# Kernel optimization log

Measured on AMD Instinct MI355X. Metric: run time of the kernel, lower is better.

Reference implementation:

```python
import jax, jax.numpy as jnp
import numpy as np

H = 8          # num_attention_heads
HEAD_DIM = 24  # 192 / 8


def setup_inputs() -> dict:
    key = jax.random.key(0)
    k1, k2, k3 = jax.random.split(key, 3)
    B, S, D = 4, 2048, 192
    x = jax.random.normal(k1, (B, S, D), dtype=jnp.float32)
    mask0 = jnp.zeros((B, 1, 1, S), dtype=jnp.float32)  # HF additive attention mask
    w_attn = jax.random.normal(k2, (D, 3 * D), dtype=jnp.float32) * 0.02
    b_attn = jnp.zeros((3 * D,), dtype=jnp.float32)
    w_proj = jax.random.normal(k3, (D, D), dtype=jnp.float32) * 0.02
    b_proj = jnp.zeros((D,), dtype=jnp.float32)
    return {"x": x, "mask0": mask0, "w_attn": w_attn, "b_attn": b_attn,
            "w_proj": w_proj, "b_proj": b_proj}


def reference(x, mask0, w_attn, b_attn, w_proj, b_proj):
    B, S, D = x.shape
    # fused QKV projection (GPT2 Conv1D: x @ W + b)
    qkv = x @ w_attn + b_attn                       # [B,S,3D]
    q, k, v = jnp.split(qkv, 3, axis=-1)
    def split_heads(t):
        return t.reshape(B, S, H, HEAD_DIM).transpose(0, 2, 1, 3)  # [B,H,S,hd]
    q, k, v = split_heads(q), split_heads(k), split_heads(v)
    # scaled QK^T
    scores = jnp.einsum('bhqd,bhkd->bhqk', q, k) / jnp.sqrt(
        jnp.asarray(HEAD_DIM, dtype=q.dtype))
    # causal mask (masked_fill with dtype min), then additive padding mask
    causal = jnp.tril(jnp.ones((S, S), dtype=bool))
    mask_value = jnp.finfo(scores.dtype).min
    scores = jnp.where(causal, scores, mask_value) + mask0
    attn = jax.nn.softmax(scores, axis=-1)          # [B,H,S,S]
    # attn_dropout is identity in eval mode
    out = jnp.einsum('bhqk,bhkd->bhqd', attn, v)    # [B,H,S,hd]
    out = out.transpose(0, 2, 1, 3).reshape(B, S, D)
    return out @ w_proj + b_proj
```

## Files before the change

### kernel.cpp

```cpp
#include <hip/hip_runtime.h>

typedef unsigned short u16;
typedef unsigned int u32;
typedef __bf16 bf16x8 __attribute__((ext_vector_type(8)));
typedef float f32x4 __attribute__((ext_vector_type(4)));
typedef float f32x16 __attribute__((ext_vector_type(16)));
typedef u32 u32x2 __attribute__((ext_vector_type(2)));
typedef u32 u32x4 __attribute__((ext_vector_type(4)));

#define NB 4
#define NS 2048
#define ND 192
#define NH 8
#define HD 24
#define NM (NB*NS)
#define N3 (3*ND)
#define NBH (NB*NH)
#define NROWS (NBH*NS)

#define LOG2E 1.4426950408889634f
#define QSCALE (0.20412414523193152f * 1.4426950408889634f)

__device__ __forceinline__ u16 f2bf(float f){
  union { float f; unsigned u; } a; a.f = f;
  unsigned r = a.u + 0x7fffu + ((a.u >> 16) & 1u);
  return (u16)(r >> 16);
}
__device__ __forceinline__ float b2f(u16 h){
  union { u32 u; float f; } a; a.u = ((u32)h) << 16; return a.f;
}
__device__ __forceinline__ u32 cvtpk(float lo, float hi){
  u32 r; asm("v_cvt_pk_bf16_f32 %0, %1, %2" : "=v"(r) : "v"(lo), "v"(hi)); return r;
}
__device__ __forceinline__ void pswap(u32 &a, u32 &b){
  asm("v_permlane32_swap_b32 %0, %1" : "+v"(a), "+v"(b));
}

__device__ __forceinline__ void transpose64(
    const float* __restrict__ src, int srcN, u16* __restrict__ dst, int dstK,
    int k0, int n0, u16 (*sh)[68], int tid)
{
  int r = tid >> 2, cs = tid & 3;
  const float* sp = src + (size_t)(k0 + r)*srcN + n0 + cs*16;
  #pragma unroll
  for (int q = 0; q < 4; ++q) {
    float4 v = *(const float4*)(sp + q*4);
    u16 o[4] = { f2bf(v.x), f2bf(v.y), f2bf(v.z), f2bf(v.w) };
    *(u32x2*)&sh[r][cs*16 + q*4] = *(const u32x2*)o;
  }
  __syncthreads();
  int n = tid >> 2, ks = tid & 3;
  u16 tmp[16];
  #pragma unroll
  for (int j = 0; j < 16; ++j) tmp[j] = sh[ks*16 + j][n];
  u16* dp = dst + (size_t)(n0 + n)*dstK + k0 + ks*16;
  *(u32x4*)dp       = *(const u32x4*)tmp;
  *(u32x4*)(dp + 8) = *(const u32x4*)(tmp + 8);
}

__global__ __launch_bounds__(256) void prep_kernel(
    const float* __restrict__ w_attn, const float* __restrict__ w_proj,
    u16* __restrict__ wta, u16* __restrict__ wtp)
{
  __shared__ u16 sh[64][68];
  const int bid = blockIdx.x, tid = threadIdx.x;
  if (bid < 27) {
    int kt = bid/9, nt = bid%9;
    transpose64(w_attn, N3, wta, ND, kt*64, nt*64, sh, tid);
  } else {
    int t = bid - 27; int kt = t/3, nt = t%3;
    transpose64(w_proj, ND, wtp, ND, kt*64, nt*64, sh, tid);
  }
}

__global__ __launch_bounds__(256) void qkv_kernel(
    const float* __restrict__ x, const u16* __restrict__ wta,
    const float* __restrict__ b_attn, const float* __restrict__ mask0,
    u16* __restrict__ qp, u16* __restrict__ kp, u16* __restrict__ vtp)
{
  __shared__ u16 tile[96*72];
  const int m0 = blockIdx.x*64, n0 = blockIdx.y*96;
  const int tid = threadIdx.x;
  const int w = tid >> 6, lane = tid & 63, c = lane & 15, g = lane >> 4;
  f32x4 acc[6] = {};
  const int ar = m0 + w*16 + c;
  const float* xrow = x + (size_t)ar*ND;
  #pragma unroll
  for (int ks = 0; ks < 6; ++ks) {
    float4 xa = *(const float4*)(xrow + ks*32 + g*8);
    float4 xc = *(const float4*)(xrow + ks*32 + g*8 + 4);
    union { u32 wrd[4]; bf16x8 v; } afu;
    afu.wrd[0] = cvtpk(xa.x, xa.y); afu.wrd[1] = cvtpk(xa.z, xa.w);
    afu.wrd[2] = cvtpk(xc.x, xc.y); afu.wrd[3] = cvtpk(xc.z, xc.w);
    bf16x8 af = afu.v;
    #pragma unroll
    for (int t = 0; t < 6; ++t) {
      bf16x8 bfr = *(const bf16x8*)(wta + (size_t)(n0 + t*16 + c)*ND + ks*32 + g*8);
      acc[t] = __builtin_amdgcn_mfma_f32_16x16x32_bf16(af, bfr, acc[t], 0, 0, 0);
    }
  }
  const int b = m0 >> 11, sb = m0 & (NS-1);
  if (n0 >= 384) {
    const int h0 = (n0 - 384)/HD;
    #pragma unroll
    for (int t = 0; t < 6; ++t) {
      float bias = b_attn[n0 + t*16 + c];
      #pragma unroll
      for (int r = 0; r < 4; ++r)
        tile[(t*16 + c)*72 + w*16 + g*4 + r] = f2bf(acc[t][r] + bias);
    }
    __syncthreads();
    if (tid < 200) {
      int row = tid >> 1, seg = tid & 1;
      if (row < 96) {
        int hl = row / HD, dv = row % HD;
        u16* dst = vtp + ((size_t)((b*NH + h0 + hl)*32 + dv))*NS + sb + seg*32;
        const u16* src = &tile[row*72 + seg*32];
        #pragma unroll
        for (int q = 0; q < 4; ++q)
          *(u32x4*)(dst + q*8) = *(const u32x4*)(src + q*8);
      } else {
        int hl = row - 96;
        u16* dst = vtp + ((size_t)((b*NH + h0 + hl)*32 + 24))*NS + sb + seg*32;
        u16 ones[8] = {0x3F80,0x3F80,0x3F80,0x3F80,0x3F80,0x3F80,0x3F80,0x3F80};
        #pragma unroll
        for (int q = 0; q < 4; ++q)
          *(u32x4*)(dst + q*8) = *(const u32x4*)ones;
      }
    }
  } else {
    const bool isQ = (n0 < 192);
    const float scl = isQ ? QSCALE : 1.0f;
    #pragma unroll
    for (int t = 0; t < 6; ++t) {
      float bias = b_attn[n0 + t*16 + c];
      #pragma unroll
      for (int r = 0; r < 4; ++r)
        tile[(w*16 + g*4 + r)*104 + t*16 + c] = f2bf((acc[t][r] + bias)*scl);
    }
    __syncthreads();
    int row = tid >> 2, run = tid & 3;
    int h0 = (n0 % 192)/HD;
    u16 d24 = isQ ? (u16)0x3F80
                  : f2bf(mask0[b*NS + sb + row] * LOG2E);
    const u16* src = &tile[row*104 + run*24];
    union { u32x4 q[4]; u16 s[32]; } buf;
    buf.q[0] = *(const u32x4*)(src);
    buf.q[1] = *(const u32x4*)(src + 8);
    buf.q[2] = *(const u32x4*)(src + 16);
    buf.s[24] = d24;
    #pragma unroll
    for (int j = 25; j < 32; ++j) buf.s[j] = 0;
    u16* dst = (isQ ? qp : kp)
             + ((size_t)((b*NS + sb + row)*NH + h0 + run))*32;
    #pragma unroll
    for (int q = 0; q < 4; ++q)
      *(u32x4*)(dst + q*8) = buf.q[q];
  }
}

__global__ __launch_bounds__(256) void attn_kernel(
    const u16* __restrict__ qp, const u16* __restrict__ kp,
    const u16* __restrict__ vtp, u16* __restrict__ po, float* __restrict__ pmf)
{
  __shared__ u16 klds[2][64][40];
  __shared__ u16 vlds[2][32][72];

  const int bh = blockIdx.x;
  const int g  = 15 - (int)blockIdx.y;
  const int part = blockIdx.z;
  const int b = bh >> 3, h = bh & 7;
  const int tid = threadIdx.x;
  const int w = tid >> 6, lane = tid & 63, c = lane & 31, hi = lane >> 5;
  const int q0 = g*128 + w*32;
  const int t0 = part ? g + 1 : 0;
  const int ntp = g + 1;

  const size_t rowstride = NH*32;
  const size_t qkbase = (size_t)b*NS*rowstride + h*32;

  const u16* qrow = qp + qkbase + (size_t)(q0 + c)*rowstride;
  bf16x8 qf0 = *(const bf16x8*)(qrow + hi*8);
  bf16x8 qf1 = *(const bf16x8*)(qrow + 16 + hi*8);

  const int krow = tid >> 2, kch = tid & 3;
  const int vrow = tid >> 3, vch = tid & 7;
  const u16* kgsrc = kp + qkbase + (size_t)(t0*64 + krow)*rowstride + kch*8;
  const u16* vgsrc = vtp + ((size_t)(bh*32 + vrow))*NS + t0*64 + vch*8;

  u32x4 kreg = *(const u32x4*)(kgsrc);
  u32x4 vreg = *(const u32x4*)(vgsrc);
  *(u32x4*)&klds[0][krow][kch*8] = kreg;
  *(u32x4*)&vlds[0][vrow][vch*8] = vreg;
  __syncthreads();

  f32x16 o = {0};
  const f32x16 z16 = {0};
  float m = 0.f;

  for (int dt = 0; dt < ntp; ++dt) {
    const int cur = dt & 1;
    if (dt + 1 < ntp) {
      kreg = *(const u32x4*)(kgsrc + (size_t)(dt+1)*64*rowstride);
      vreg = *(const u32x4*)(vgsrc + (dt+1)*64);
    }
    const int kb0 = (t0 + dt)*64;
    if (kb0 <= q0) {
      const bool a1 = (kb0 + 32 <= q0);
      bf16x8 ka0 = *(const bf16x8*)&klds[cur][c][hi*8];
      bf16x8 ka1 = *(const bf16x8*)&klds[cur][c][16 + hi*8];
      __builtin_amdgcn_s_setprio(1);
      f32x16 st = __builtin_amdgcn_mfma_f32_32x32x16_bf16(ka0, qf0, z16, 0, 0, 0);
      st        = __builtin_amdgcn_mfma_f32_32x32x16_bf16(ka1, qf1, st,  0, 0, 0);
      __builtin_amdgcn_s_setprio(0);
      f32x16 su;
      if (a1) {
        bf16x8 kb0f = *(const bf16x8*)&klds[cur][32 + c][hi*8];
        bf16x8 kb1f = *(const bf16x8*)&klds[cur][32 + c][16 + hi*8];
        __builtin_amdgcn_s_setprio(1);
        su = __builtin_amdgcn_mfma_f32_32x32x16_bf16(kb0f, qf0, z16, 0, 0, 0);
        su = __builtin_amdgcn_mfma_f32_32x32x16_bf16(kb1f, qf1, su,  0, 0, 0);
        __builtin_amdgcn_s_setprio(0);
      }
      float pm = -3.0e38f;
      if (kb0 == q0) {
        #pragma unroll
        for (int r = 0; r < 16; ++r) {
          int krel = (r & 3) + 8*(r >> 2) + 4*hi;
          float s = (krel > c) ? -3.0e38f : st[r];
          st[r] = s; pm = fmaxf(pm, s);
        }
      } else {
        #pragma unroll
        for (int r = 0; r < 16; ++r) pm = fmaxf(pm, st[r]);
      }
      if (a1) {
        if (kb0 + 32 == q0) {
          #pragma unroll
          for (int r = 0; r < 16; ++r) {
            int krel = (r & 3) + 8*(r >> 2) + 4*hi;
            float s = (krel > c) ? -3.0e38f : su[r];
            su[r] = s; pm = fmaxf(pm, s);
          }
        } else {
          #pragma unroll
          for (int r = 0; r < 16; ++r) pm = fmaxf(pm, su[r]);
        }
      }
      if (!__all(pm - m <= 8.f)) {
        float pm2 = fmaxf(pm, __shfl_xor(pm, 32));
        float mn = fmaxf(m, pm2);
        float al = __builtin_amdgcn_exp2f(m - mn);
        #pragma unroll
        for (int r = 0; r < 16; ++r) o[r] *= al;
        m = mn;
      }
      #pragma unroll
      for (int r = 0; r < 16; ++r) st[r] = __builtin_amdgcn_exp2f(st[r] - m);
      if (a1) {
        #pragma unroll
        for (int r = 0; r < 16; ++r) su[r] = __builtin_amdgcn_exp2f(su[r] - m);
      }
      {
        u32 a0 = cvtpk(st[0], st[1]),  b0 = cvtpk(st[4], st[5]);
        u32 a1w = cvtpk(st[2], st[3]), b1 = cvtpk(st[6], st[7]);
        pswap(a0, b0); pswap(a1w, b1);
        u32 a2 = cvtpk(st[8], st[9]),  b2 = cvtpk(st[12], st[13]);
        u32 a3 = cvtpk(st[10], st[11]), b3 = cvtpk(st[14], st[15]);
        pswap(a2, b2); pswap(a3, b3);
        union { u32 wrd[4]; bf16x8 v; } pf0, pf1;
        pf0.wrd[0] = a0; pf0.wrd[1] = a1w; pf0.wrd[2] = b0; pf0.wrd[3] = b1;
        pf1.wrd[0] = a2; pf1.wrd[1] = a3;  pf1.wrd[2] = b2; pf1.wrd[3] = b3;
        bf16x8 va0 = *(const bf16x8*)&vlds[cur][c][hi*8];
        bf16x8 va1 = *(const bf16x8*)&vlds[cur][c][16 + hi*8];
        __builtin_amdgcn_s_setprio(1);
        o = __builtin_amdgcn_mfma_f32_32x32x16_bf16(va0, pf0.v, o, 0, 0, 0);
        o = __builtin_amdgcn_mfma_f32_32x32x16_bf16(va1, pf1.v, o, 0, 0, 0);
        __builtin_amdgcn_s_setprio(0);
      }
      if (a1) {
        u32 a0 = cvtpk(su[0], su[1]),  b0 = cvtpk(su[4], su[5]);
        u32 a1w = cvtpk(su[2], su[3]), b1 = cvtpk(su[6], su[7]);
        pswap(a0, b0); pswap(a1w, b1);
        u32 a2 = cvtpk(su[8], su[9]),  b2 = cvtpk(su[12], su[13]);
        u32 a3 = cvtpk(su[10], su[11]), b3 = cvtpk(su[14], su[15]);
        pswap(a2, b2); pswap(a3, b3);
        union { u32 wrd[4]; bf16x8 v; } pf0, pf1;
        pf0.wrd[0] = a0; pf0.wrd[1] = a1w; pf0.wrd[2] = b0; pf0.wrd[3] = b1;
        pf1.wrd[0] = a2; pf1.wrd[1] = a3;  pf1.wrd[2] = b2; pf1.wrd[3] = b3;
        bf16x8 va0 = *(const bf16x8*)&vlds[cur][c][32 + hi*8];
        bf16x8 va1 = *(const bf16x8*)&vlds[cur][c][48 + hi*8];
        __builtin_amdgcn_s_setprio(1);
        o = __builtin_amdgcn_mfma_f32_32x32x16_bf16(va0, pf0.v, o, 0, 0, 0);
        o = __builtin_amdgcn_mfma_f32_32x32x16_bf16(va1, pf1.v, o, 0, 0, 0);
        __builtin_amdgcn_s_setprio(0);
      }
    }
    if (dt + 1 < ntp) {
      *(u32x4*)&klds[cur^1][krow][kch*8] = kreg;
      *(u32x4*)&vlds[cur^1][vrow][vch*8] = vreg;
    }
    __syncthreads();
  }

  const int pidx = part*NROWS + bh*NS + q0 + c;
  u16* porow = po + (size_t)pidx*32;
  #pragma unroll
  for (int rr = 0; rr < 4; ++rr) {
    u32 lo = cvtpk(o[rr*4 + 0], o[rr*4 + 1]);
    u32 h2 = cvtpk(o[rr*4 + 2], o[rr*4 + 3]);
    u32x2 wv = {lo, h2};
    *(u32x2*)(porow + rr*8 + hi*4) = wv;
  }
  if (hi == 0) pmf[pidx] = (t0*64 <= q0) ? m : -3.0e38f;
}

__global__ __launch_bounds__(256) void merge_kernel(
    const u16* __restrict__ po, const float* __restrict__ pmf,
    u16* __restrict__ ao)
{
  int i = blockIdx.x*256 + threadIdx.x;
  int bh = i >> 11, q = i & (NS-1);
  int b = bh >> 3, h = bh & 7;
  float m1 = pmf[i], m2 = pmf[NROWS + i];
  float M = fmaxf(m1, m2);
  float w1 = __builtin_amdgcn_exp2f(m1 - M);
  float w2 = __builtin_amdgcn_exp2f(m2 - M);
  const u16* r1 = po + (size_t)i*32;
  const u16* r2 = r1 + (size_t)NROWS*32;
  u16 a1[32], a2[32];
  #pragma unroll
  for (int q4 = 0; q4 < 4; ++q4) {
    *(u32x4*)(a1 + q4*8) = *(const u32x4*)(r1 + q4*8);
    *(u32x4*)(a2 + q4*8) = *(const u32x4*)(r2 + q4*8);
  }
  float l = b2f(a1[24])*w1 + b2f(a2[24])*w2;
  float inv = 1.0f / l;
  u16 ob[24];
  #pragma unroll
  for (int d = 0; d < 24; ++d)
    ob[d] = f2bf((b2f(a1[d])*w1 + b2f(a2[d])*w2)*inv);
  u16* dst = ao + ((size_t)(b*NS + q))*ND + h*HD;
  #pragma unroll
  for (int q4 = 0; q4 < 3; ++q4)
    *(u32x4*)(dst + q4*8) = *(const u32x4*)(ob + q4*8);
}

__global__ __launch_bounds__(256) void proj_kernel(
    const u16* __restrict__ ao, const u16* __restrict__ wtp,
    const float* __restrict__ bp, float* __restrict__ out)
{
  const int m0 = blockIdx.x*64, n0 = blockIdx.y*64;
  const int tid = threadIdx.x;
  const int w = tid >> 6, lane = tid & 63, c = lane & 15, g = lane >> 4;
  f32x4 acc[4] = {};
  const int ar = m0 + w*16 + c;
  #pragma unroll
  for (int ks = 0; ks < 6; ++ks) {
    bf16x8 af = *(const bf16x8*)(ao + (size_t)ar*ND + ks*32 + g*8);
    #pragma unroll
    for (int t = 0; t < 4; ++t) {
      bf16x8 bfr = *(const bf16x8*)(wtp + (size_t)(n0 + t*16 + c)*ND + ks*32 + g*8);
      acc[t] = __builtin_amdgcn_mfma_f32_16x16x32_bf16(af, bfr, acc[t], 0, 0, 0);
    }
  }
  #pragma unroll
  for (int t = 0; t < 4; ++t) {
    int n = n0 + t*16 + c;
    float bias = bp[n];
    #pragma unroll
    for (int r = 0; r < 4; ++r) {
      int mm = m0 + w*16 + g*4 + r;
      out[(size_t)mm*ND + n] = acc[t][r] + bias;
    }
  }
}

extern "C" void kernel_launch(void* const* d_in, const int* in_sizes, int n_in,
                              void* d_out, int out_size, void* d_ws, size_t ws_size,
                              hipStream_t stream)
{
  const float* x      = (const float*)d_in[0];
  const float* mask0  = (const float*)d_in[1];
  const float* w_attn = (const float*)d_in[2];
  const float* b_attn = (const float*)d_in[3];
  const float* w_proj = (const float*)d_in[4];
  const float* b_proj = (const float*)d_in[5];
  float* out = (float*)d_out;

  char* ws = (char*)d_ws;
  u16*   qp  = (u16*)(ws);
  u16*   kp  = (u16*)(ws + ((size_t)4  << 20));
  u16*   vtp = (u16*)(ws + ((size_t)8  << 20));
  u16*   wta = (u16*)(ws + ((size_t)12 << 20));
  u16*   wtp = (u16*)(ws + ((size_t)12 << 20) + 256*1024);
  u16*   ao  = (u16*)(ws + ((size_t)12 << 20) + 512*1024);
  u16*   po  = (u16*)(ws + ((size_t)16 << 20));
  float* pmf = (float*)(ws + ((size_t)24 << 20));

  prep_kernel<<<36, 256, 0, stream>>>(w_attn, w_proj, wta, wtp);
  qkv_kernel<<<dim3(NM/64, 6), 256, 0, stream>>>(x, wta, b_attn, mask0,
                                                 qp, kp, vtp);
  attn_kernel<<<dim3(NBH, 16, 2), 256, 0, stream>>>(qp, kp, vtp, po, pmf);
  merge_kernel<<<256, 256, 0, stream>>>(po, pmf, ao);
  proj_kernel<<<dim3(NM/64, ND/64), 256, 0, stream>>>(ao, wtp, b_proj, out);
}
```

Before: 133.9 us.

## Split attention KV range into four balanced partitions and merge four partials

Each query block's causal key range is now divided evenly into four parts instead of two halves, and the attention grid launches four partitions along z. This gives more blocks and shorter per-block loops, aiming to improve load balance and occupancy across CUs. The merge kernel now combines four partial results with log-sum-exp weights. In exchange it adds more partial-output traffic and merge work, and some blocks with small g get no tiles and only write sentinel values.

New measurement: 133.9 us. No clear change (+0.0%).

```diff
diff --git a/kernel.cpp b/kernel.cpp
--- a/kernel.cpp
+++ b/kernel.cpp
@@ -17,6 +17,7 @@
 #define N3 (3*ND)
 #define NBH (NB*NH)
 #define NROWS (NBH*NS)
+#define NPART 4
 
 #define LOG2E 1.4426950408889634f
 #define QSCALE (0.20412414523193152f * 1.4426950408889634f)
@@ -173,8 +174,10 @@
   const int tid = threadIdx.x;
   const int w = tid >> 6, lane = tid & 63, c = lane & 31, hi = lane >> 5;
   const int q0 = g*128 + w*32;
-  const int t0 = part ? g + 1 : 0;
-  const int ntp = g + 1;
+  const int nt = 2*g + 2;
+  const int base = nt >> 2, rem = nt & 3;
+  const int cnt = base + (part < rem ? 1 : 0);
+  const int t0 = part*base + (part < rem ? part : rem);
 
   const size_t rowstride = NH*32;
   const size_t qkbase = (size_t)b*NS*rowstride + h*32;
@@ -188,119 +191,121 @@
   const u16* kgsrc = kp + qkbase + (size_t)(t0*64 + krow)*rowstride + kch*8;
   const u16* vgsrc = vtp + ((size_t)(bh*32 + vrow))*NS + t0*64 + vch*8;
 
-  u32x4 kreg = *(const u32x4*)(kgsrc);
-  u32x4 vreg = *(const u32x4*)(vgsrc);
-  *(u32x4*)&klds[0][krow][kch*8] = kreg;
-  *(u32x4*)&vlds[0][vrow][vch*8] = vreg;
-  __syncthreads();
-
   f32x16 o = {0};
   const f32x16 z16 = {0};
   float m = 0.f;
 
-  for (int dt = 0; dt < ntp; ++dt) {
-    const int cur = dt & 1;
-    if (dt + 1 < ntp) {
-      kreg = *(const u32x4*)(kgsrc + (size_t)(dt+1)*64*rowstride);
-      vreg = *(const u32x4*)(vgsrc + (dt+1)*64);
-    }
-    const int kb0 = (t0 + dt)*64;
-    if (kb0 <= q0) {
-      const bool a1 = (kb0 + 32 <= q0);
-      bf16x8 ka0 = *(const bf16x8*)&klds[cur][c][hi*8];
-      bf16x8 ka1 = *(const bf16x8*)&klds[cur][c][16 + hi*8];
-      __builtin_amdgcn_s_setprio(1);
-      f32x16 st = __builtin_amdgcn_mfma_f32_32x32x16_bf16(ka0, qf0, z16, 0, 0, 0);
-      st        = __builtin_amdgcn_mfma_f32_32x32x16_bf16(ka1, qf1, st,  0, 0, 0);
-      __builtin_amdgcn_s_setprio(0);
-      f32x16 su;
-      if (a1) {
-        bf16x8 kb0f = *(const bf16x8*)&klds[cur][32 + c][hi*8];
-        bf16x8 kb1f = *(const bf16x8*)&klds[cur][32 + c][16 + hi*8];
+  if (cnt > 0) {
+    u32x4 kreg = *(const u32x4*)(kgsrc);
+    u32x4 vreg = *(const u32x4*)(vgsrc);
+    *(u32x4*)&klds[0][krow][kch*8] = kreg;
+    *(u32x4*)&vlds[0][vrow][vch*8] = vreg;
+    __syncthreads();
+
+    for (int dt = 0; dt < cnt; ++dt) {
+      const int cur = dt & 1;
+      if (dt + 1 < cnt) {
+        kreg = *(const u32x4*)(kgsrc + (size_t)(dt+1)*64*rowstride);
+        vreg = *(const u32x4*)(vgsrc + (dt+1)*64);
+      }
+      const int kb0 = (t0 + dt)*64;
+      if (kb0 <= q0) {
+        const bool a1 = (kb0 + 32 <= q0);
+        bf16x8 ka0 = *(const bf16x8*)&klds[cur][c][hi*8];
+        bf16x8 ka1 = *(const bf16x8*)&klds[cur][c][16 + hi*8];
         __builtin_amdgcn_s_setprio(1);
-        su = __builtin_amdgcn_mfma_f32_32x32x16_bf16(kb0f, qf0, z16, 0, 0, 0);
-        su = __builtin_amdgcn_mfma_f32_32x32x16_bf16(kb1f, qf1, su,  0, 0, 0);
+        f32x16 st = __builtin_amdgcn_mfma_f32_32x32x16_bf16(ka0, qf0, z16, 0, 0, 0);
+        st        = __builtin_amdgcn_mfma_f32_32x32x16_bf16(ka1, qf1, st,  0, 0, 0);
         __builtin_amdgcn_s_setprio(0);
-      }
-      float pm = -3.0e38f;
-      if (kb0 == q0) {
-        #pragma unroll
-        for (int r = 0; r < 16; ++r) {
-          int krel = (r & 3) + 8*(r >> 2) + 4*hi;
-          float s = (krel > c) ? -3.0e38f : st[r];
-          st[r] = s; pm = fmaxf(pm, s);
-        }
-      } else {
-        #pragma unroll
-        for (int r = 0; r < 16; ++r) pm = fmaxf(pm, st[r]);
-      }
-      if (a1) {
-        if (kb0 + 32 == q0) {
+        f32x16 su;
+        if (a1) {
+          bf16x8 kb0f = *(const bf16x8*)&klds[cur][32 + c][hi*8];
+          bf16x8 kb1f = *(const bf16x8*)&klds[cur][32 + c][16 + hi*8];
+          __builtin_amdgcn_s_setprio(1);
+          su = __builtin_amdgcn_mfma_f32_32x32x16_bf16(kb0f, qf0, z16, 0, 0, 0);
+          su = __builtin_amdgcn_mfma_f32_32x32x16_bf16(kb1f, qf1, su,  0, 0, 0);
+          __builtin_amdgcn_s_setprio(0);
+        }
+        float pm = -3.0e38f;
+        if (kb0 == q0) {
           #pragma unroll
           for (int r = 0; r < 16; ++r) {
             int krel = (r & 3) + 8*(r >> 2) + 4*hi;
-            float s = (krel > c) ? -3.0e38f : su[r];
-            su[r] = s; pm = fmaxf(pm, s);
+            float s = (krel > c) ? -3.0e38f : st[r];
+            st[r] = s; pm = fmaxf(pm, s);
           }
         } else {
           #pragma unroll
-          for (int r = 0; r < 16; ++r) pm = fmaxf(pm, su[r]);
+          for (int r = 0; r < 16; ++r) pm = fmaxf(pm, st[r]);
+        }
+        if (a1) {
+          if (kb0 + 32 == q0) {
+            #pragma unroll
+            for (int r = 0; r < 16; ++r) {
+              int krel = (r & 3) + 8*(r >> 2) + 4*hi;
+              float s = (krel > c) ? -3.0e38f : su[r];
+              su[r] = s; pm = fmaxf(pm, s);
+            }
+          } else {
+            #pragma unroll
+            for (int r = 0; r < 16; ++r) pm = fmaxf(pm, su[r]);
+          }
+        }
+        if (!__all(pm - m <= 8.f)) {
+          float pm2 = fmaxf(pm, __shfl_xor(pm, 32));
+          float mn = fmaxf(m, pm2);
+          float al = __builtin_amdgcn_exp2f(m - mn);
+          #pragma unroll
+          for (int r = 0; r < 16; ++r) o[r] *= al;
+          m = mn;
+        }
+        #pragma unroll
+        for (int r = 0; r < 16; ++r) st[r] = __builtin_amdgcn_exp2f(st[r] - m);
+        if (a1) {
+          #pragma unroll
+          for (int r = 0; r < 16; ++r) su[r] = __builtin_amdgcn_exp2f(su[r] - m);
+        }
+        {
+          u32 a0 = cvtpk(st[0], st[1]),  b0 = cvtpk(st[4], st[5]);
+          u32 a1w = cvtpk(st[2], st[3]), b1 = cvtpk(st[6], st[7]);
+          pswap(a0, b0); pswap(a1w, b1);
+          u32 a2 = cvtpk(st[8], st[9]),  b2 = cvtpk(st[12], st[13]);
+          u32 a3 = cvtpk(st[10], st[11]), b3 = cvtpk(st[14], st[15]);
+          pswap(a2, b2); pswap(a3, b3);
+          union { u32 wrd[4]; bf16x8 v; } pf0, pf1;
+          pf0.wrd[0] = a0; pf0.wrd[1] = a1w; pf0.wrd[2] = b0; pf0.wrd[3] = b1;
+          pf1.wrd[0] = a2; pf1.wrd[1] = a3;  pf1.wrd[2] = b2; pf1.wrd[3] = b3;
+          bf16x8 va0 = *(const bf16x8*)&vlds[cur][c][hi*8];
+          bf16x8 va1 = *(const bf16x8*)&vlds[cur][c][16 + hi*8];
+          __builtin_amdgcn_s_setprio(1);
+          o = __builtin_amdgcn_mfma_f32_32x32x16_bf16(va0, pf0.v, o, 0, 0, 0);
+          o = __builtin_amdgcn_mfma_f32_32x32x16_bf16(va1, pf1.v, o, 0, 0, 0);
+          __builtin_amdgcn_s_setprio(0);
+        }
+        if (a1) {
+          u32 a0 = cvtpk(su[0], su[1]),  b0 = cvtpk(su[4], su[5]);
+          u32 a1w = cvtpk(su[2], su[3]), b1 = cvtpk(su[6], su[7]);
+          pswap(a0, b0); pswap(a1w, b1);
+          u32 a2 = cvtpk(su[8], su[9]),  b2 = cvtpk(su[12], su[13]);
+          u32 a3 = cvtpk(su[10], su[11]), b3 = cvtpk(su[14], su[15]);
+          pswap(a2, b2); pswap(a3, b3);
+          union { u32 wrd[4]; bf16x8 v; } pf0, pf1;
+          pf0.wrd[0] = a0; pf0.wrd[1] = a1w; pf0.wrd[2] = b0; pf0.wrd[3] = b1;
+          pf1.wrd[0] = a2; pf1.wrd[1] = a3;  pf1.wrd[2] = b2; pf1.wrd[3] = b3;
+          bf16x8 va0 = *(const bf16x8*)&vlds[cur][c][32 + hi*8];
+          bf16x8 va1 = *(const bf16x8*)&vlds[cur][c][48 + hi*8];
+          __builtin_amdgcn_s_setprio(1);
+          o = __builtin_amdgcn_mfma_f32_32x32x16_bf16(va0, pf0.v, o, 0, 0, 0);
+          o = __builtin_amdgcn_mfma_f32_32x32x16_bf16(va1, pf1.v, o, 0, 0, 0);
+          __builtin_amdgcn_s_setprio(0);
         }
       }
-      if (!__all(pm - m <= 8.f)) {
-        float pm2 = fmaxf(pm, __shfl_xor(pm, 32));
-        float mn = fmaxf(m, pm2);
-        float al = __builtin_amdgcn_exp2f(m - mn);
-        #pragma unroll
-        for (int r = 0; r < 16; ++r) o[r] *= al;
-        m = mn;
+      if (dt + 1 < cnt) {
+        *(u32x4*)&klds[cur^1][krow][kch*8] = kreg;
+        *(u32x4*)&vlds[cur^1][vrow][vch*8] = vreg;
       }
-      #pragma unroll
-      for (int r = 0; r < 16; ++r) st[r] = __builtin_amdgcn_exp2f(st[r] - m);
-      if (a1) {
-        #pragma unroll
-        for (int r = 0; r < 16; ++r) su[r] = __builtin_amdgcn_exp2f(su[r] - m);
-      }
-      {
-        u32 a0 = cvtpk(st[0], st[1]),  b0 = cvtpk(st[4], st[5]);
-        u32 a1w = cvtpk(st[2], st[3]), b1 = cvtpk(st[6], st[7]);
-        pswap(a0, b0); pswap(a1w, b1);
-        u32 a2 = cvtpk(st[8], st[9]),  b2 = cvtpk(st[12], st[13]);
-        u32 a3 = cvtpk(st[10], st[11]), b3 = cvtpk(st[14], st[15]);
-        pswap(a2, b2); pswap(a3, b3);
-        union { u32 wrd[4]; bf16x8 v; } pf0, pf1;
-        pf0.wrd[0] = a0; pf0.wrd[1] = a1w; pf0.wrd[2] = b0; pf0.wrd[3] = b1;
-        pf1.wrd[0] = a2; pf1.wrd[1] = a3;  pf1.wrd[2] = b2; pf1.wrd[3] = b3;
-        bf16x8 va0 = *(const bf16x8*)&vlds[cur][c][hi*8];
-        bf16x8 va1 = *(const bf16x8*)&vlds[cur][c][16 + hi*8];
-        __builtin_amdgcn_s_setprio(1);
-        o = __builtin_amdgcn_mfma_f32_32x32x16_bf16(va0, pf0.v, o, 0, 0, 0);
-        o = __builtin_amdgcn_mfma_f32_32x32x16_bf16(va1, pf1.v, o, 0, 0, 0);
-        __builtin_amdgcn_s_setprio(0);
-      }
-      if (a1) {
-        u32 a0 = cvtpk(su[0], su[1]),  b0 = cvtpk(su[4], su[5]);
-        u32 a1w = cvtpk(su[2], su[3]), b1 = cvtpk(su[6], su[7]);
-        pswap(a0, b0); pswap(a1w, b1);
-        u32 a2 = cvtpk(su[8], su[9]),  b2 = cvtpk(su[12], su[13]);
-        u32 a3 = cvtpk(su[10], su[11]), b3 = cvtpk(su[14], su[15]);
-        pswap(a2, b2); pswap(a3, b3);
-        union { u32 wrd[4]; bf16x8 v; } pf0, pf1;
-        pf0.wrd[0] = a0; pf0.wrd[1] = a1w; pf0.wrd[2] = b0; pf0.wrd[3] = b1;
-        pf1.wrd[0] = a2; pf1.wrd[1] = a3;  pf1.wrd[2] = b2; pf1.wrd[3] = b3;
-        bf16x8 va0 = *(const bf16x8*)&vlds[cur][c][32 + hi*8];
-        bf16x8 va1 = *(const bf16x8*)&vlds[cur][c][48 + hi*8];
-        __builtin_amdgcn_s_setprio(1);
-        o = __builtin_amdgcn_mfma_f32_32x32x16_bf16(va0, pf0.v, o, 0, 0, 0);
-        o = __builtin_amdgcn_mfma_f32_32x32x16_bf16(va1, pf1.v, o, 0, 0, 0);
-        __builtin_amdgcn_s_setprio(0);
-      }
-    }
-    if (dt + 1 < ntp) {
-      *(u32x4*)&klds[cur^1][krow][kch*8] = kreg;
-      *(u32x4*)&vlds[cur^1][vrow][vch*8] = vreg;
-    }
-    __syncthreads();
+      __syncthreads();
+    }
   }
 
   const int pidx = part*NROWS + bh*NS + q0 + c;
@@ -312,7 +317,7 @@
     u32x2 wv = {lo, h2};
     *(u32x2*)(porow + rr*8 + hi*4) = wv;
   }
-  if (hi == 0) pmf[pidx] = (t0*64 <= q0) ? m : -3.0e38f;
+  if (hi == 0) pmf[pidx] = (cnt > 0 && t0*64 <= q0) ? m : -3.0e38f;
 }
 
 __global__ __launch_bounds__(256) void merge_kernel(
@@ -322,24 +327,25 @@
   int i = blockIdx.x*256 + threadIdx.x;
   int bh = i >> 11, q = i & (NS-1);
   int b = bh >> 3, h = bh & 7;
-  float m1 = pmf[i], m2 = pmf[NROWS + i];
-  float M = fmaxf(m1, m2);
-  float w1 = __builtin_amdgcn_exp2f(m1 - M);
-  float w2 = __builtin_amdgcn_exp2f(m2 - M);
-  const u16* r1 = po + (size_t)i*32;
-  const u16* r2 = r1 + (size_t)NROWS*32;
-  u16 a1[32], a2[32];
-  #pragma unroll
-  for (int q4 = 0; q4 < 4; ++q4) {
-    *(u32x4*)(a1 + q4*8) = *(const u32x4*)(r1 + q4*8);
-    *(u32x4*)(a2 + q4*8) = *(const u32x4*)(r2 + q4*8);
-  }
-  float l = b2f(a1[24])*w1 + b2f(a2[24])*w2;
-  float inv = 1.0f / l;
+  float mp[NPART];
+  float M = -3.0e38f;
+  #pragma unroll
+  for (int p = 0; p < NPART; ++p) { mp[p] = pmf[p*NROWS + i]; M = fmaxf(M, mp[p]); }
+  float acc[25] = {};
+  #pragma unroll
+  for (int p = 0; p < NPART; ++p) {
+    float wp = __builtin_amdgcn_exp2f(mp[p] - M);
+    const u16* rp = po + ((size_t)p*NROWS + i)*32;
+    u16 a[32];
+    #pragma unroll
+    for (int q4 = 0; q4 < 4; ++q4) *(u32x4*)(a + q4*8) = *(const u32x4*)(rp + q4*8);
+    #pragma unroll
+    for (int d = 0; d < 25; ++d) acc[d] += b2f(a[d])*wp;
+  }
+  float inv = 1.0f / acc[24];
   u16 ob[24];
   #pragma unroll
-  for (int d = 0; d < 24; ++d)
-    ob[d] = f2bf((b2f(a1[d])*w1 + b2f(a2[d])*w2)*inv);
+  for (int d = 0; d < 24; ++d) ob[d] = f2bf(acc[d]*inv);
   u16* dst = ao + ((size_t)(b*NS + q))*ND + h*HD;
   #pragma unroll
   for (int q4 = 0; q4 < 3; ++q4)
@@ -396,12 +402,12 @@
   u16*   wtp = (u16*)(ws + ((size_t)12 << 20) + 256*1024);
   u16*   ao  = (u16*)(ws + ((size_t)12 << 20) + 512*1024);
   u16*   po  = (u16*)(ws + ((size_t)16 << 20));
-  float* pmf = (float*)(ws + ((size_t)24 << 20));
+  float* pmf = (float*)(ws + ((size_t)32 << 20));
 
   prep_kernel<<<36, 256, 0, stream>>>(w_attn, w_proj, wta, wtp);
   qkv_kernel<<<dim3(NM/64, 6), 256, 0, stream>>>(x, wta, b_attn, mask0,
                                                  qp, kp, vtp);
-  attn_kernel<<<dim3(NBH, 16, 2), 256, 0, stream>>>(qp, kp, vtp, po, pmf);
+  attn_kernel<<<dim3(NBH, 16, NPART), 256, 0, stream>>>(qp, kp, vtp, po, pmf);
   merge_kernel<<<256, 256, 0, stream>>>(po, pmf, ao);
   proj_kernel<<<dim3(NM/64, ND/64), 256, 0, stream>>>(ao, wtp, b_proj, out);
 }
```

## Fuse split-KV merge into projection GEMM and make Q/K head-major

Applied to the files above, without the earlier changes.

Removes the separate merge kernel: the projection kernel now reads both partial attention outputs and their row maxima, combines them and normalises while building its A fragments, so the intermediate ao buffer and one launch go away. Q and K are stored head-major ([b,h,s,32]), which makes the attention kernel's K tile loads contiguous instead of strided by NH*32. The V transpose store is reorganised so all 256 threads each write one 16-byte chunk. The trade-off is redundant merge arithmetic: each of the three column blocks of the projection repeats the merge for its rows.

Measured after the change: 130.4 us, median of 2. 1.03x faster.

```diff
diff --git a/kernel.cpp b/kernel.cpp
--- a/kernel.cpp
+++ b/kernel.cpp
@@ -17,6 +17,7 @@
 #define N3 (3*ND)
 #define NBH (NB*NH)
 #define NROWS (NBH*NS)
+#define NPART 2
 
 #define LOG2E 1.4426950408889634f
 #define QSCALE (0.20412414523193152f * 1.4426950408889634f)
@@ -110,22 +111,19 @@
         tile[(t*16 + c)*72 + w*16 + g*4 + r] = f2bf(acc[t][r] + bias);
     }
     __syncthreads();
-    if (tid < 200) {
-      int row = tid >> 1, seg = tid & 1;
+    const int chunk = tid & 7;
+    u16 ones[8] = {0x3F80,0x3F80,0x3F80,0x3F80,0x3F80,0x3F80,0x3F80,0x3F80};
+    #pragma unroll
+    for (int rr = 0; rr < 4; ++rr) {
+      int row = rr*32 + (tid >> 3);
       if (row < 96) {
-        int hl = row / HD, dv = row % HD;
-        u16* dst = vtp + ((size_t)((b*NH + h0 + hl)*32 + dv))*NS + sb + seg*32;
-        const u16* src = &tile[row*72 + seg*32];
-        #pragma unroll
-        for (int q = 0; q < 4; ++q)
-          *(u32x4*)(dst + q*8) = *(const u32x4*)(src + q*8);
-      } else {
+        int hl = row/HD, dv = row - hl*HD;
+        u16* dst = vtp + ((size_t)((b*NH + h0 + hl)*32 + dv))*NS + sb + chunk*8;
+        *(u32x4*)dst = *(const u32x4*)&tile[row*72 + chunk*8];
+      } else if (row < 100) {
         int hl = row - 96;
-        u16* dst = vtp + ((size_t)((b*NH + h0 + hl)*32 + 24))*NS + sb + seg*32;
-        u16 ones[8] = {0x3F80,0x3F80,0x3F80,0x3F80,0x3F80,0x3F80,0x3F80,0x3F80};
-        #pragma unroll
-        for (int q = 0; q < 4; ++q)
-          *(u32x4*)(dst + q*8) = *(const u32x4*)ones;
+        u16* dst = vtp + ((size_t)((b*NH + h0 + hl)*32 + 24))*NS + sb + chunk*8;
+        *(u32x4*)dst = *(const u32x4*)ones;
       }
     }
   } else {
@@ -152,7 +150,7 @@
     #pragma unroll
     for (int j = 25; j < 32; ++j) buf.s[j] = 0;
     u16* dst = (isQ ? qp : kp)
-             + ((size_t)((b*NS + sb + row)*NH + h0 + run))*32;
+             + ((size_t)((b*NH + h0 + run)*NS) + sb + row)*32;
     #pragma unroll
     for (int q = 0; q < 4; ++q)
       *(u32x4*)(dst + q*8) = buf.q[q];
@@ -169,24 +167,26 @@
   const int bh = blockIdx.x;
   const int g  = 15 - (int)blockIdx.y;
   const int part = blockIdx.z;
-  const int b = bh >> 3, h = bh & 7;
   const int tid = threadIdx.x;
   const int w = tid >> 6, lane = tid & 63, c = lane & 31, hi = lane >> 5;
   const int q0 = g*128 + w*32;
-  const int t0 = part ? g + 1 : 0;
-  const int ntp = g + 1;
-
-  const size_t rowstride = NH*32;
-  const size_t qkbase = (size_t)b*NS*rowstride + h*32;
-
-  const u16* qrow = qp + qkbase + (size_t)(q0 + c)*rowstride;
+  const int cnt = g + 1;
+  const int t0 = part*cnt;
+
+  const size_t qkbase = (size_t)bh*NS*32;
+
+  const u16* qrow = qp + qkbase + (size_t)(q0 + c)*32;
   bf16x8 qf0 = *(const bf16x8*)(qrow + hi*8);
   bf16x8 qf1 = *(const bf16x8*)(qrow + 16 + hi*8);
 
   const int krow = tid >> 2, kch = tid & 3;
   const int vrow = tid >> 3, vch = tid & 7;
-  const u16* kgsrc = kp + qkbase + (size_t)(t0*64 + krow)*rowstride + kch*8;
+  const u16* kgsrc = kp + qkbase + (size_t)(t0*64 + krow)*32 + kch*8;
   const u16* vgsrc = vtp + ((size_t)(bh*32 + vrow))*NS + t0*64 + vch*8;
+
+  f32x16 o = {0};
+  const f32x16 z16 = {0};
+  float m = 0.f;
 
   u32x4 kreg = *(const u32x4*)(kgsrc);
   u32x4 vreg = *(const u32x4*)(vgsrc);
@@ -194,14 +194,10 @@
   *(u32x4*)&vlds[0][vrow][vch*8] = vreg;
   __syncthreads();
 
-  f32x16 o = {0};
-  const f32x16 z16 = {0};
-  float m = 0.f;
-
-  for (int dt = 0; dt < ntp; ++dt) {
+  for (int dt = 0; dt < cnt; ++dt) {
     const int cur = dt & 1;
-    if (dt + 1 < ntp) {
-      kreg = *(const u32x4*)(kgsrc + (size_t)(dt+1)*64*rowstride);
+    if (dt + 1 < cnt) {
+      kreg = *(const u32x4*)(kgsrc + (size_t)(dt+1)*64*32);
       vreg = *(const u32x4*)(vgsrc + (dt+1)*64);
     }
     const int kb0 = (t0 + dt)*64;
@@ -296,7 +292,7 @@
         __builtin_amdgcn_s_setprio(0);
       }
     }
-    if (dt + 1 < ntp) {
+    if (dt + 1 < cnt) {
       *(u32x4*)&klds[cur^1][krow][kch*8] = kreg;
       *(u32x4*)&vlds[cur^1][vrow][vch*8] = vreg;
     }
@@ -315,53 +311,52 @@
   if (hi == 0) pmf[pidx] = (t0*64 <= q0) ? m : -3.0e38f;
 }
 
-__global__ __launch_bounds__(256) void merge_kernel(
+__global__ __launch_bounds__(256) void proj_kernel(
     const u16* __restrict__ po, const float* __restrict__ pmf,
-    u16* __restrict__ ao)
-{
-  int i = blockIdx.x*256 + threadIdx.x;
-  int bh = i >> 11, q = i & (NS-1);
-  int b = bh >> 3, h = bh & 7;
-  float m1 = pmf[i], m2 = pmf[NROWS + i];
-  float M = fmaxf(m1, m2);
-  float w1 = __builtin_amdgcn_exp2f(m1 - M);
-  float w2 = __builtin_amdgcn_exp2f(m2 - M);
-  const u16* r1 = po + (size_t)i*32;
-  const u16* r2 = r1 + (size_t)NROWS*32;
-  u16 a1[32], a2[32];
-  #pragma unroll
-  for (int q4 = 0; q4 < 4; ++q4) {
-    *(u32x4*)(a1 + q4*8) = *(const u32x4*)(r1 + q4*8);
-    *(u32x4*)(a2 + q4*8) = *(const u32x4*)(r2 + q4*8);
-  }
-  float l = b2f(a1[24])*w1 + b2f(a2[24])*w2;
-  float inv = 1.0f / l;
-  u16 ob[24];
-  #pragma unroll
-  for (int d = 0; d < 24; ++d)
-    ob[d] = f2bf((b2f(a1[d])*w1 + b2f(a2[d])*w2)*inv);
-  u16* dst = ao + ((size_t)(b*NS + q))*ND + h*HD;
-  #pragma unroll
-  for (int q4 = 0; q4 < 3; ++q4)
-    *(u32x4*)(dst + q4*8) = *(const u32x4*)(ob + q4*8);
-}
-
-__global__ __launch_bounds__(256) void proj_kernel(
-    const u16* __restrict__ ao, const u16* __restrict__ wtp,
-    const float* __restrict__ bp, float* __restrict__ out)
+    const u16* __restrict__ wtp, const float* __restrict__ bp,
+    float* __restrict__ out)
 {
   const int m0 = blockIdx.x*64, n0 = blockIdx.y*64;
   const int tid = threadIdx.x;
   const int w = tid >> 6, lane = tid & 63, c = lane & 15, g = lane >> 4;
+  const int ar = m0 + w*16 + c;
+  const int b = ar >> 11, s = ar & (NS-1);
+
+  bf16x8 af[6];
+  #pragma unroll
+  for (int ks = 0; ks < 6; ++ks) {
+    int ch = ks*32 + g*8;
+    int h = ch / HD, dd = ch - h*HD;
+    size_t ridx = (size_t)(b*NH + h)*NS + s;
+    float m1 = pmf[ridx], m2 = pmf[NROWS + ridx];
+    float M = fmaxf(m1, m2);
+    float w1 = __builtin_amdgcn_exp2f(m1 - M);
+    float w2 = __builtin_amdgcn_exp2f(m2 - M);
+    const u16* r1 = po + ridx*32;
+    const u16* r2 = po + ((size_t)NROWS + ridx)*32;
+    u32x4 pa = *(const u32x4*)(r1 + dd);
+    u32x4 pb = *(const u32x4*)(r2 + dd);
+    float l = b2f(r1[24])*w1 + b2f(r2[24])*w2;
+    float inv = 1.0f / l;
+    float s1 = w1*inv, s2 = w2*inv;
+    union { u32 wrd[4]; bf16x8 v; } fu;
+    #pragma unroll
+    for (int jj = 0; jj < 4; ++jj) {
+      u32 wa = pa[jj], wb = pb[jj];
+      float v0 = b2f((u16)(wa & 0xffff))*s1 + b2f((u16)(wb & 0xffff))*s2;
+      float v1 = b2f((u16)(wa >> 16))*s1 + b2f((u16)(wb >> 16))*s2;
+      fu.wrd[jj] = cvtpk(v0, v1);
+    }
+    af[ks] = fu.v;
+  }
+
   f32x4 acc[4] = {};
-  const int ar = m0 + w*16 + c;
   #pragma unroll
   for (int ks = 0; ks < 6; ++ks) {
-    bf16x8 af = *(const bf16x8*)(ao + (size_t)ar*ND + ks*32 + g*8);
     #pragma unroll
     for (int t = 0; t < 4; ++t) {
       bf16x8 bfr = *(const bf16x8*)(wtp + (size_t)(n0 + t*16 + c)*ND + ks*32 + g*8);
-      acc[t] = __builtin_amdgcn_mfma_f32_16x16x32_bf16(af, bfr, acc[t], 0, 0, 0);
+      acc[t] = __builtin_amdgcn_mfma_f32_16x16x32_bf16(af[ks], bfr, acc[t], 0, 0, 0);
     }
   }
   #pragma unroll
@@ -394,14 +389,12 @@
   u16*   vtp = (u16*)(ws + ((size_t)8  << 20));
   u16*   wta = (u16*)(ws + ((size_t)12 << 20));
   u16*   wtp = (u16*)(ws + ((size_t)12 << 20) + 256*1024);
-  u16*   ao  = (u16*)(ws + ((size_t)12 << 20) + 512*1024);
-  u16*   po  = (u16*)(ws + ((size_t)16 << 20));
-  float* pmf = (float*)(ws + ((size_t)24 << 20));
+  u16*   po  = (u16*)(ws + ((size_t)13 << 20));
+  float* pmf = (float*)(ws + ((size_t)21 << 20));
 
   prep_kernel<<<36, 256, 0, stream>>>(w_attn, w_proj, wta, wtp);
   qkv_kernel<<<dim3(NM/64, 6), 256, 0, stream>>>(x, wta, b_attn, mask0,
                                                  qp, kp, vtp);
-  attn_kernel<<<dim3(NBH, 16, 2), 256, 0, stream>>>(qp, kp, vtp, po, pmf);
-  merge_kernel<<<256, 256, 0, stream>>>(po, pmf, ao);
-  proj_kernel<<<dim3(NM/64, ND/64), 256, 0, stream>>>(ao, wtp, b_proj, out);
-}
+  attn_kernel<<<dim3(NBH, 16, NPART), 256, 0, stream>>>(qp, kp, vtp, po, pmf);
+  proj_kernel<<<dim3(NM/64, ND/64), 256, 0, stream>>>(po, pmf, wtp, b_proj, out);
+}
```
